# Optimization experiments

Measured on AMD Instinct MI355X. Metric: run time of the kernel, lower is better.

Reference implementation:

```python
import jax, jax.numpy as jnp
import numpy as np

B, C_IN, C_OUT, N, K = 16, 128, 128, 4096, 16


def setup_inputs() -> dict:
    key = jax.random.key(0)
    k1, k2, k3, k4 = jax.random.split(key, 4)
    x = jax.random.normal(k1, (B, C_IN, N, 1), dtype=jnp.float32)
    edge_index = jax.random.randint(k2, (2, B, N, K), 0, N, dtype=jnp.int32)
    # 1x1 conv weight of BasicConv([C_IN, C_OUT], 'relu', None, bias=False)
    W = jax.random.normal(k3, (C_OUT, C_IN), dtype=jnp.float32) * (1.0 / np.sqrt(C_IN))
    # module bias param, initialized to zeros; use random here to exercise the add
    bias = jax.random.normal(k4, (1, C_OUT, 1, 1), dtype=jnp.float32) * 0.01
    return {"x": x, "edge_index": edge_index, "W": W, "bias": bias}


def reference(x, edge_index, W, bias):
    b, _, n, _ = x.shape
    # BasicConv: 1x1 conv (no bias) + ReLU
    h = jax.nn.relu(jnp.einsum('oi,binu->bonu', W, x))  # [B, C_out, N, 1]
    h2 = h[..., 0]                                       # [B, C_out, N]
    # add_self_loops: append self index along neighbor dim
    self_idx = jnp.broadcast_to(jnp.arange(n, dtype=edge_index.dtype)[None, None, :, None],
                                (2, b, n, 1))
    ei = jnp.concatenate([edge_index, self_idx], axis=-1)  # [2, B, N, K+1]
    idx = ei[0]                                            # [B, N, K+1]
    deg = ei.shape[-1]
    norm = 1.0 / deg
    # batched_index_select: gather neighbor features -> [B, C_out, N, K+1]
    x_j = jax.vmap(lambda hb, ib: hb[:, ib])(h2, idx)
    aggr = (x_j * norm).sum(axis=-1, keepdims=True)        # [B, C_out, N, 1]
    return aggr + bias
```

## Files before the change

### kernel.cpp

```cpp
#include <hip/hip_runtime.h>

#define B_    16
#define CIN_  128
#define COUT_ 128
#define N_    4096
#define K_    16

typedef __attribute__((ext_vector_type(8))) _Float16 f16x8;
typedef __attribute__((ext_vector_type(2))) _Float16 f16x2;
typedef __attribute__((ext_vector_type(2))) __fp16   h16x2;
typedef __attribute__((ext_vector_type(4))) float f32x4;
typedef __attribute__((ext_vector_type(4))) int   i32x4;

__device__ inline f16x2 pkrtz(float a, float b) {
  union { h16x2 r; f16x2 f; } u;
  u.r = __builtin_amdgcn_cvt_pkrtz(a, b);
  return u.f;
}
__device__ inline unsigned h2u(f16x2 h) {
  union { f16x2 h; unsigned u; } x; x.h = h; return x.u;
}
__device__ inline f16x2 u2h(unsigned u) {
  union { unsigned u; f16x2 h; } x; x.u = u; return x.h;
}
__device__ inline unsigned short f2h(float f) {
  _Float16 h = (_Float16)f;
  union { _Float16 h; unsigned short u; } x; x.h = h; return x.u;
}

__global__ __launch_bounds__(1024, 4) void gemm_relu_k(
    const float* __restrict__ W, const float* __restrict__ x,
    unsigned short* __restrict__ h) {
  __shared__ unsigned short Wl[128 * 136];
  __shared__ unsigned short He[256 * 144];
  const int tid  = threadIdx.x;
  const int l    = blockIdx.x;
  const int slot = l >> 3;
  const int b    = ((l & 7) << 1) | (slot >> 4);
  const int n0   = (slot & 15) * 256;

#pragma unroll
  for (int r = 0; r < 2; ++r) {
    int id  = tid + 1024 * r;
    int co  = id >> 4;
    int seg = id & 15;
    const float4* wp = reinterpret_cast<const float4*>(W + co * CIN_ + 8 * seg);
    float4 v0 = wp[0];
    float4 v1 = wp[1];
    f16x2 q0 = pkrtz(v0.x, v0.y);
    f16x2 q1 = pkrtz(v0.z, v0.w);
    f16x2 q2 = pkrtz(v1.x, v1.y);
    f16x2 q3 = pkrtz(v1.z, v1.w);
    *reinterpret_cast<uint4*>(&Wl[co * 136 + 8 * seg]) =
        make_uint4(h2u(q0), h2u(q1), h2u(q2), h2u(q3));
  }

  const int lane = tid & 63;
  const int w    = tid >> 6;
  const int m    = lane & 15;
  const int quad = lane >> 4;

  const float* xb = x + (size_t)b * CIN_ * N_ + n0 + 16 * w + m;
  f16x8 a[4];
#pragma unroll
  for (int s = 0; s < 4; ++s)
#pragma unroll
    for (int jj = 0; jj < 4; ++jj) {
      float e0 = xb[(size_t)(32 * s + 8 * quad + 2 * jj)     * N_];
      float e1 = xb[(size_t)(32 * s + 8 * quad + 2 * jj + 1) * N_];
      f16x2 p = pkrtz(e0, e1);
      a[s][2 * jj]     = p[0];
      a[s][2 * jj + 1] = p[1];
    }

  __syncthreads();

  const int nrow = 16 * w + 4 * quad;
#pragma unroll
  for (int t = 0; t < 8; ++t) {
    f32x4 c = {0.f, 0.f, 0.f, 0.f};
#pragma unroll
    for (int s = 0; s < 4; ++s) {
      f16x8 bf = *reinterpret_cast<const f16x8*>(
          &Wl[(16 * t + m) * 136 + 32 * s + 8 * quad]);
      c = __builtin_amdgcn_mfma_f32_16x16x32_f16(a[s], bf, c, 0, 0, 0);
    }
    int co = 16 * t + m;
#pragma unroll
    for (int r = 0; r < 4; ++r) {
      float v = c[r] > 0.f ? c[r] : 0.f;
      He[(nrow + r) * 144 + co] = f2h(v);
    }
  }
  __syncthreads();

  unsigned short* hb = h + ((size_t)b * N_ + n0) * COUT_;
  const int seg = tid & 15;
  const int nr  = tid >> 4;
#pragma unroll
  for (int p = 0; p < 4; ++p) {
    int n = nr + 64 * p;
    uint4 v = *reinterpret_cast<const uint4*>(&He[n * 144 + 8 * seg]);
    *reinterpret_cast<uint4*>(hb + (size_t)n * COUT_ + 8 * seg) = v;
  }
}

__global__ __launch_bounds__(256, 4) void aggr_k(
    const unsigned short* __restrict__ h, const int* __restrict__ ei,
    const float* __restrict__ bias, float* __restrict__ out) {
  __shared__ int idx_t[17 * 64];
  const int tid  = threadIdx.x;
  const int l    = blockIdx.x;
  const int rest = l >> 3;
  const int b    = ((l & 7) << 1) | (rest >> 6);
  const int n0   = (rest & 63) * 64;

  {
    int n  = tid >> 2;
    int kq = tid & 3;
    i32x4 v = __builtin_nontemporal_load(
        reinterpret_cast<const i32x4*>(ei + ((size_t)b * N_ + n0 + n) * K_) + kq);
    idx_t[(4 * kq + 0) * 64 + n] = v.x;
    idx_t[(4 * kq + 1) * 64 + n] = v.y;
    idx_t[(4 * kq + 2) * 64 + n] = v.z;
    idx_t[(4 * kq + 3) * 64 + n] = v.w;
    if (tid < 64) idx_t[16 * 64 + tid] = n0 + tid;
  }
  __syncthreads();

  const int q = tid & 15;
  const int g = tid >> 4;
  const unsigned short* hb = h + (size_t)b * N_ * COUT_;

  f16x2 acc2[4][4];
#pragma unroll
  for (int j = 0; j < 4; ++j)
#pragma unroll
    for (int d = 0; d < 4; ++d) acc2[j][d] = (f16x2)(_Float16)0;

#pragma unroll 2
  for (int k = 0; k < 17; ++k) {
    uint4 v[4];
#pragma unroll
    for (int j = 0; j < 4; ++j) {
      int node = idx_t[k * 64 + 4 * g + j];
      v[j] = *reinterpret_cast<const uint4*>(hb + (size_t)node * COUT_ + 8 * q);
    }
#pragma unroll
    for (int j = 0; j < 4; ++j) {
      acc2[j][0] += u2h(v[j].x);
      acc2[j][1] += u2h(v[j].y);
      acc2[j][2] += u2h(v[j].z);
      acc2[j][3] += u2h(v[j].w);
    }
  }

  const float norm = 1.0f / 17.0f;
  const float4 bv0 = *reinterpret_cast<const float4*>(bias + 8 * q);
  const float4 bv1 = *reinterpret_cast<const float4*>(bias + 8 * q + 4);
  float* ob = out + (size_t)b * COUT_ * N_ + n0 + 4 * g;
#pragma unroll
  for (int c = 0; c < 8; ++c) {
    int co = 8 * q + c;
    float bb = (c < 4) ? ((c == 0) ? bv0.x : (c == 1) ? bv0.y : (c == 2) ? bv0.z : bv0.w)
                       : ((c == 4) ? bv1.x : (c == 5) ? bv1.y : (c == 6) ? bv1.z : bv1.w);
    float4 r;
    r.x = (float)acc2[0][c >> 1][c & 1] * norm + bb;
    r.y = (float)acc2[1][c >> 1][c & 1] * norm + bb;
    r.z = (float)acc2[2][c >> 1][c & 1] * norm + bb;
    r.w = (float)acc2[3][c >> 1][c & 1] * norm + bb;
    *reinterpret_cast<float4*>(ob + (size_t)co * N_) = r;
  }
}

extern "C" void kernel_launch(void* const* d_in, const int* in_sizes, int n_in,
                              void* d_out, int out_size, void* d_ws, size_t ws_size,
                              hipStream_t stream) {
  const float* x    = (const float*)d_in[0];
  const int*   ei   = (const int*)d_in[1];
  const float* W    = (const float*)d_in[2];
  const float* bias = (const float*)d_in[3];
  float* out = (float*)d_out;
  unsigned short* h = (unsigned short*)d_ws;

  gemm_relu_k<<<dim3(256), dim3(1024), 0, stream>>>(W, x, h);
  aggr_k<<<dim3(B_ * N_ / 64), 256, 0, stream>>>(h, ei, bias, out);
}
```

Before: 113.3 us.

## Write GEMM output directly via swapped MFMA operands; shrink aggregation tiles and software-pipeline gathers

```diff
diff --git a/kernel.cpp b/kernel.cpp
--- a/kernel.cpp
+++ b/kernel.cpp
@@ -23,16 +23,14 @@
 __device__ inline f16x2 u2h(unsigned u) {
   union { unsigned u; f16x2 h; } x; x.u = u; return x.h;
 }
-__device__ inline unsigned short f2h(float f) {
-  _Float16 h = (_Float16)f;
-  union { _Float16 h; unsigned short u; } x; x.h = h; return x.u;
+__device__ inline unsigned packh(float a, float b) {
+  f16x2 p; p[0] = (_Float16)a; p[1] = (_Float16)b; return h2u(p);
 }
 
 __global__ __launch_bounds__(1024, 4) void gemm_relu_k(
     const float* __restrict__ W, const float* __restrict__ x,
     unsigned short* __restrict__ h) {
   __shared__ unsigned short Wl[128 * 136];
-  __shared__ unsigned short He[256 * 144];
   const int tid  = threadIdx.x;
   const int l    = blockIdx.x;
   const int slot = l >> 3;
@@ -75,56 +73,47 @@
 
   __syncthreads();
 
-  const int nrow = 16 * w + 4 * quad;
+  unsigned short* hrow = h + ((size_t)b * N_ + n0 + 16 * w + m) * COUT_;
 #pragma unroll
   for (int t = 0; t < 8; ++t) {
     f32x4 c = {0.f, 0.f, 0.f, 0.f};
 #pragma unroll
     for (int s = 0; s < 4; ++s) {
-      f16x8 bf = *reinterpret_cast<const f16x8*>(
+      f16x8 wf = *reinterpret_cast<const f16x8*>(
           &Wl[(16 * t + m) * 136 + 32 * s + 8 * quad]);
-      c = __builtin_amdgcn_mfma_f32_16x16x32_f16(a[s], bf, c, 0, 0, 0);
+      c = __builtin_amdgcn_mfma_f32_16x16x32_f16(wf, a[s], c, 0, 0, 0);
     }
-    int co = 16 * t + m;
-#pragma unroll
-    for (int r = 0; r < 4; ++r) {
-      float v = c[r] > 0.f ? c[r] : 0.f;
-      He[(nrow + r) * 144 + co] = f2h(v);
-    }
-  }
-  __syncthreads();
-
-  unsigned short* hb = h + ((size_t)b * N_ + n0) * COUT_;
-  const int seg = tid & 15;
-  const int nr  = tid >> 4;
-#pragma unroll
-  for (int p = 0; p < 4; ++p) {
-    int n = nr + 64 * p;
-    uint4 v = *reinterpret_cast<const uint4*>(&He[n * 144 + 8 * seg]);
-    *reinterpret_cast<uint4*>(hb + (size_t)n * COUT_ + 8 * seg) = v;
+    float r0 = c[0] > 0.f ? c[0] : 0.f;
+    float r1 = c[1] > 0.f ? c[1] : 0.f;
+    float r2 = c[2] > 0.f ? c[2] : 0.f;
+    float r3 = c[3] > 0.f ? c[3] : 0.f;
+    *reinterpret_cast<uint2*>(hrow + 16 * t + 4 * quad) =
+        make_uint2(packh(r0, r1), packh(r2, r3));
   }
 }
 
-__global__ __launch_bounds__(256, 4) void aggr_k(
+__global__ __launch_bounds__(256, 8) void aggr_k(
     const unsigned short* __restrict__ h, const int* __restrict__ ei,
     const float* __restrict__ bias, float* __restrict__ out) {
-  __shared__ int idx_t[17 * 64];
+  __shared__ int idx_t[17 * 32];
   const int tid  = threadIdx.x;
   const int l    = blockIdx.x;
   const int rest = l >> 3;
-  const int b    = ((l & 7) << 1) | (rest >> 6);
-  const int n0   = (rest & 63) * 64;
+  const int b    = ((l & 7) << 1) | (rest >> 7);
+  const int n0   = (rest & 127) * 32;
 
   {
-    int n  = tid >> 2;
-    int kq = tid & 3;
-    i32x4 v = __builtin_nontemporal_load(
-        reinterpret_cast<const i32x4*>(ei + ((size_t)b * N_ + n0 + n) * K_) + kq);
-    idx_t[(4 * kq + 0) * 64 + n] = v.x;
-    idx_t[(4 * kq + 1) * 64 + n] = v.y;
-    idx_t[(4 * kq + 2) * 64 + n] = v.z;
-    idx_t[(4 * kq + 3) * 64 + n] = v.w;
-    if (tid < 64) idx_t[16 * 64 + tid] = n0 + tid;
+    if (tid < 128) {
+      int n  = tid >> 2;
+      int kq = tid & 3;
+      i32x4 v = __builtin_nontemporal_load(
+          reinterpret_cast<const i32x4*>(ei + ((size_t)b * N_ + n0 + n) * K_) + kq);
+      idx_t[(4 * kq + 0) * 32 + n] = v.x;
+      idx_t[(4 * kq + 1) * 32 + n] = v.y;
+      idx_t[(4 * kq + 2) * 32 + n] = v.z;
+      idx_t[(4 * kq + 3) * 32 + n] = v.w;
+    }
+    if (tid < 32) idx_t[16 * 32 + tid] = n0 + tid;
   }
   __syncthreads();
 
@@ -132,44 +121,55 @@
   const int g = tid >> 4;
   const unsigned short* hb = h + (size_t)b * N_ * COUT_;
 
-  f16x2 acc2[4][4];
+  f16x2 acc2[2][4];
 #pragma unroll
-  for (int j = 0; j < 4; ++j)
+  for (int jj = 0; jj < 2; ++jj)
 #pragma unroll
-    for (int d = 0; d < 4; ++d) acc2[j][d] = (f16x2)(_Float16)0;
+    for (int d = 0; d < 4; ++d) acc2[jj][d] = (f16x2)(_Float16)0;
 
-#pragma unroll 2
-  for (int k = 0; k < 17; ++k) {
-    uint4 v[4];
+#define LDK(K, V)                                                          \
+  {                                                                        \
+    int na_ = idx_t[(K) * 32 + 2 * g];                                     \
+    int nb_ = idx_t[(K) * 32 + 2 * g + 1];                                 \
+    V[0] = *reinterpret_cast<const uint4*>(hb + (size_t)na_ * COUT_ + 8 * q); \
+    V[1] = *reinterpret_cast<const uint4*>(hb + (size_t)nb_ * COUT_ + 8 * q); \
+  }
+#define ACCK(V)                                                            \
+  {                                                                        \
+    _Pragma("unroll")                                                      \
+    for (int jj = 0; jj < 2; ++jj) {                                       \
+      acc2[jj][0] += u2h(V[jj].x);                                         \
+      acc2[jj][1] += u2h(V[jj].y);                                         \
+      acc2[jj][2] += u2h(V[jj].z);                                         \
+      acc2[jj][3] += u2h(V[jj].w);                                         \
+    }                                                                      \
+  }
+
+  uint4 va[2], vb[2];
+  LDK(0, va);
 #pragma unroll
-    for (int j = 0; j < 4; ++j) {
-      int node = idx_t[k * 64 + 4 * g + j];
-      v[j] = *reinterpret_cast<const uint4*>(hb + (size_t)node * COUT_ + 8 * q);
-    }
-#pragma unroll
-    for (int j = 0; j < 4; ++j) {
-      acc2[j][0] += u2h(v[j].x);
-      acc2[j][1] += u2h(v[j].y);
-      acc2[j][2] += u2h(v[j].z);
-      acc2[j][3] += u2h(v[j].w);
-    }
+  for (int k = 0; k < 17; k += 2) {
+    if (k + 1 < 17) LDK(k + 1, vb);
+    ACCK(va);
+    if (k + 2 < 17) LDK(k + 2, va);
+    if (k + 1 < 17) ACCK(vb);
   }
+#undef LDK
+#undef ACCK
 
   const float norm = 1.0f / 17.0f;
   const float4 bv0 = *reinterpret_cast<const float4*>(bias + 8 * q);
   const float4 bv1 = *reinterpret_cast<const float4*>(bias + 8 * q + 4);
-  float* ob = out + (size_t)b * COUT_ * N_ + n0 + 4 * g;
+  float* ob = out + (size_t)b * COUT_ * N_ + n0 + 2 * g;
 #pragma unroll
   for (int c = 0; c < 8; ++c) {
     int co = 8 * q + c;
     float bb = (c < 4) ? ((c == 0) ? bv0.x : (c == 1) ? bv0.y : (c == 2) ? bv0.z : bv0.w)
                        : ((c == 4) ? bv1.x : (c == 5) ? bv1.y : (c == 6) ? bv1.z : bv1.w);
-    float4 r;
+    float2 r;
     r.x = (float)acc2[0][c >> 1][c & 1] * norm + bb;
     r.y = (float)acc2[1][c >> 1][c & 1] * norm + bb;
-    r.z = (float)acc2[2][c >> 1][c & 1] * norm + bb;
-    r.w = (float)acc2[3][c >> 1][c & 1] * norm + bb;
-    *reinterpret_cast<float4*>(ob + (size_t)co * N_) = r;
+    *reinterpret_cast<float2*>(ob + (size_t)co * N_) = r;
   }
 }
 
@@ -184,5 +184,5 @@
   unsigned short* h = (unsigned short*)d_ws;
 
   gemm_relu_k<<<dim3(256), dim3(1024), 0, stream>>>(W, x, h);
-  aggr_k<<<dim3(B_ * N_ / 64), 256, 0, stream>>>(h, ei, bias, out);
+  aggr_k<<<dim3(2048), dim3(256), 0, stream>>>(h, ei, bias, out);
 }
```

Measured after the change: 116.5 us. 2.9% more time.
